# Kernel tuning notes

Hardware: AMD Instinct MI355X
Metric: run time of the kernel (lower is better)

## Reference

```python
import jax, jax.numpy as jnp
import numpy as np

B, N = 4, 1024
D_MODEL, N_HEADS, D_HEAD, D_COORD = 512, 8, 64, 2


def setup_inputs() -> dict:
    key = jax.random.key(0)
    ks = jax.random.split(key, 8)
    sd = 1.0 / np.sqrt(D_MODEL)
    return {
        "x": jax.random.normal(ks[0], (B, N, D_MODEL), dtype=jnp.float32),
        "positions": jax.random.uniform(ks[1], (N, D_COORD), dtype=jnp.float32) * 32.0,
        "W_Q": jax.random.normal(ks[2], (D_MODEL, N_HEADS * D_HEAD), dtype=jnp.float32) * sd,
        "W_K": jax.random.normal(ks[3], (D_MODEL, N_HEADS * D_HEAD), dtype=jnp.float32) * sd,
        "W_V": jax.random.normal(ks[4], (D_MODEL, N_HEADS * D_HEAD), dtype=jnp.float32) * sd,
        "W_O": jax.random.normal(ks[5], (N_HEADS * D_HEAD, D_MODEL), dtype=jnp.float32) * sd,
        "U": jax.random.normal(ks[6], (N_HEADS, D_HEAD, D_HEAD), dtype=jnp.float32),
        "freqs": jax.random.normal(ks[7], (N_HEADS, D_HEAD // 2, D_COORD), dtype=jnp.float32),
    }


def reference(x, positions, W_Q, W_K, W_V, W_O, U, freqs):
    # x: (B,N,d_model); positions: (N,d_coord); U: (H,dh,dh); freqs: (H,m,d_coord)
    Bn, Nn, _ = x.shape
    H, dh, _ = U.shape
    m = dh // 2
    scale = (dh // 2) ** -0.5

    Q = (x @ W_Q).reshape(Bn, Nn, H, dh)
    K = (x @ W_K).reshape(Bn, Nn, H, dh)
    V = (x @ W_V).reshape(Bn, Nn, H, dh)

    # Active-subspace projector: Pi = qr(U)[0] @ qr(U)[0].T per head
    Uq = jax.vmap(lambda u: jnp.linalg.qr(u)[0])(U)              # (H,dh,dh)
    P = jnp.einsum('hde,hfe->hdf', Uq, Uq)                       # U U^T
    Qp = jnp.einsum('bnhd,hdf->bhnf', Q, P)                      # (B,H,N,dh)
    Kp = jnp.einsum('bnhd,hdf->bhnf', K, P)

    # Relative rotation: R_rel(r_j - r_i) is block-diag 2x2 rotations with
    # angle theta_ijm = freqs_m . (r_j - r_i) = a_jm - a_im (separable), so
    # q^T R(r_j-r_i) k = (R(a_i)q)^T (R(a_j)k)  -- exact RoPE identity.
    ang = jnp.einsum('nc,hmc->hnm', positions, freqs)            # (H,N,m)
    c = jnp.cos(ang)[None]                                       # (1,H,N,m)
    s = jnp.sin(ang)[None]

    def rot(v):  # v: (B,H,N,dh) -> rotated (even, odd) halves (B,H,N,m)
        ve, vo = v[..., ::2], v[..., 1::2]
        return ve * c - vo * s, ve * s + vo * c

    qe, qo = rot(Qp)
    ke, ko = rot(Kp)
    scores = (jnp.einsum('bhim,bhjm->bhij', qe, ke)
              + jnp.einsum('bhim,bhjm->bhij', qo, ko)) * scale   # (B,H,N,N)
    w = jax.nn.softmax(scores, axis=-1)
    out = jnp.einsum('bhij,bjhd->bihd', w, V).reshape(Bn, Nn, H * dh)
    return out @ W_O
```

## Files before the change

### kernel.cpp

```cpp
#include <hip/hip_runtime.h>
#include <hip/hip_bf16.h>
#include <math.h>

#define NBATCH 4
#define NSEQ   1024
#define DMODEL 512
#define NH     8
#define DH     64
#define MROWS  (NBATCH*NSEQ)
#define MHALF  (DH/2)

typedef __attribute__((ext_vector_type(8))) short bf16x8;
typedef __attribute__((ext_vector_type(4))) float floatx4;

__device__ __forceinline__ uint f2bf2(float lo, float hi) {
    union { __hip_bfloat162 h; uint u; } v;
    v.h = __float22bfloat162_rn(make_float2(lo, hi));
    return v.u;
}

__global__ __launch_bounds__(256) void prep_kernel(
    const float* __restrict__ pos, const float* __restrict__ freqs,
    const float* __restrict__ x,
    const float* __restrict__ Wq, const float* __restrict__ Wk,
    const float* __restrict__ Wv, const float* __restrict__ Wo,
    float* __restrict__ cosT, float* __restrict__ sinT,
    ushort* __restrict__ xb, ushort* __restrict__ Wt)
{
    __shared__ float T[64][65];
    const int bid = blockIdx.x;
    const int tid = threadIdx.x;

    if (bid < 1024) {
        int idx = bid * 256 + tid;
        int m = idx & 31;
        int n = (idx >> 5) & 1023;
        int h = idx >> 15;
        float a = pos[n*2+0] * freqs[(h*MHALF+m)*2+0]
                + pos[n*2+1] * freqs[(h*MHALF+m)*2+1];
        cosT[idx] = cosf(a);
        sinT[idx] = sinf(a);
    } else if (bid < 2048) {
        int idx = ((bid - 1024) * 256 + tid) * 8;
        float4 a = *(const float4*)&x[idx];
        float4 b = *(const float4*)&x[idx+4];
        uint4 pk;
        pk.x = f2bf2(a.x, a.y);
        pk.y = f2bf2(a.z, a.w);
        pk.z = f2bf2(b.x, b.y);
        pk.w = f2bf2(b.z, b.w);
        *(uint4*)&xb[idx] = pk;
    } else {
        int b2 = bid - 2048;
        int n0g = (b2 & 31) * 64;
        int k0  = (b2 >> 5) * 64;
        int mat = n0g >> 9;
        const float* W = (mat == 0) ? Wq : ((mat == 1) ? Wk : ((mat == 2) ? Wv : Wo));
        int n0 = n0g & 511;
        int c = tid & 63, r = tid >> 6;
        #pragma unroll
        for (int i = 0; i < 16; i++)
            T[r + i*4][c] = W[(k0 + r + i*4) * DMODEL + n0 + c];
        __syncthreads();
        int nl = tid >> 2;
        int kg = tid & 3;
        #pragma unroll
        for (int g = 0; g < 4; g++) {
            int kl = kg * 16 + g * 4;
            uint2 pk;
            pk.x = f2bf2(T[kl+0][nl], T[kl+1][nl]);
            pk.y = f2bf2(T[kl+2][nl], T[kl+3][nl]);
            *(uint2*)&Wt[(size_t)(n0g + nl) * DMODEL + k0 + kl] = pk;
        }
    }
}

__global__ __launch_bounds__(256) void qkv_gemm(
    const ushort* __restrict__ xb, const ushort* __restrict__ Wt,
    const float* __restrict__ cosT, const float* __restrict__ sinT,
    ushort* __restrict__ Qb, ushort* __restrict__ Kb, ushort* __restrict__ Vt)
{
    __shared__ __align__(16) ushort AB[2 * 64 * 72];
    ushort* As = AB;
    ushort* Bs = AB + 64 * 72;
    float (*Cs)[65] = (float(*)[65])AB;

    const int cb = blockIdx.x;
    const int rb = blockIdx.y;
    const int mat = cb >> 3;
    const int c0 = (cb & 7) * 64;
    const int r0 = rb * 64;
    const int ng0 = mat * 512 + c0;

    const int tid = threadIdx.x;
    const int w = tid >> 6, l = tid & 63;
    const int lr = l & 15, lg = l >> 4;

    const int srow = tid >> 2;
    const int scol = (tid & 3) * 16;

    floatx4 acc[4];
    #pragma unroll
    for (int nt = 0; nt < 4; nt++) acc[nt] = (floatx4){0.f,0.f,0.f,0.f};

    const ushort* pa = &xb[(size_t)(r0 + srow) * DMODEL + scol];
    const ushort* pb = &Wt[(size_t)(ng0 + srow) * DMODEL + scol];
    uint4 ra0 = *(const uint4*)pa;
    uint4 ra1 = *(const uint4*)(pa + 8);
    uint4 rb0 = *(const uint4*)pb;
    uint4 rb1 = *(const uint4*)(pb + 8);

    for (int k0 = 0; k0 < DMODEL; k0 += 64) {
        __syncthreads();
        *(uint4*)&As[srow*72 + scol]     = ra0;
        *(uint4*)&As[srow*72 + scol + 8] = ra1;
        *(uint4*)&Bs[srow*72 + scol]     = rb0;
        *(uint4*)&Bs[srow*72 + scol + 8] = rb1;
        __syncthreads();

        if (k0 + 64 < DMODEL) {
            const ushort* na = &xb[(size_t)(r0 + srow) * DMODEL + k0 + 64 + scol];
            const ushort* nb = &Wt[(size_t)(ng0 + srow) * DMODEL + k0 + 64 + scol];
            ra0 = *(const uint4*)na;
            ra1 = *(const uint4*)(na + 8);
            rb0 = *(const uint4*)nb;
            rb1 = *(const uint4*)(nb + 8);
        }

        #pragma unroll
        for (int ks = 0; ks < 2; ks++) {
            bf16x8 af = *(const bf16x8*)&As[(16*w + lr)*72 + ks*32 + lg*8];
            #pragma unroll
            for (int nt = 0; nt < 4; nt++) {
                bf16x8 bf = *(const bf16x8*)&Bs[(nt*16 + lr)*72 + ks*32 + lg*8];
                acc[nt] = __builtin_amdgcn_mfma_f32_16x16x32_bf16(af, bf, acc[nt], 0, 0, 0);
            }
        }
    }

    __syncthreads();
    #pragma unroll
    for (int nt = 0; nt < 4; nt++)
        #pragma unroll
        for (int r = 0; r < 4; r++)
            Cs[16*w + lg*4 + r][nt*16 + lr] = acc[nt][r];
    __syncthreads();

    const int tx = tid & 15, ty = tid >> 4;
    const int dbase = tx * 4;
    const int head = c0 >> 6;

    if (mat == 2) {
        int rowbase = r0 + ty * 4;
        int b = rowbase >> 10, n0 = rowbase & 1023;
        size_t vbase = (size_t)(b * NH + head) * DH;
        #pragma unroll
        for (int j = 0; j < 4; j++) {
            uint2 pk;
            pk.x = f2bf2(Cs[ty*4 + 0][tx*4 + j], Cs[ty*4 + 1][tx*4 + j]);
            pk.y = f2bf2(Cs[ty*4 + 2][tx*4 + j], Cs[ty*4 + 3][tx*4 + j]);
            *(uint2*)&Vt[(vbase + dbase + j) * NSEQ + n0] = pk;
        }
    } else {
        ushort* dst = (mat == 0) ? Qb : Kb;
        const float qs = (mat == 0) ? 0.17677669529663687f : 1.0f;
        #pragma unroll
        for (int i = 0; i < 4; i++) {
            int row = r0 + ty * 4 + i;
            int b = row >> 10, n = row & 1023;
            float v[4];
            #pragma unroll
            for (int p = 0; p < 2; p++) {
                int de = dbase + 2 * p;
                int m = de >> 1;
                float c = cosT[(head * NSEQ + n) * MHALF + m] * qs;
                float s = sinT[(head * NSEQ + n) * MHALF + m] * qs;
                float ve = Cs[ty*4 + i][tx*4 + 2*p];
                float vo = Cs[ty*4 + i][tx*4 + 2*p + 1];
                v[2*p]     = ve * c - vo * s;
                v[2*p + 1] = ve * s + vo * c;
            }
            uint2 pk;
            pk.x = f2bf2(v[0], v[1]);
            pk.y = f2bf2(v[2], v[3]);
            *(uint2*)&dst[((size_t)(b * NH + head) * NSEQ + n) * DH + dbase] = pk;
        }
    }
}

__global__ __launch_bounds__(256, 4) void attn_kernel(
    const ushort* __restrict__ Qb, const ushort* __restrict__ Kb,
    const ushort* __restrict__ Vt, ushort* __restrict__ Obb)
{
    __shared__ ushort Ks[64 * 72];
    __shared__ ushort Vs[64 * 72];
    __shared__ ushort Ps[64 * 72];

    const int tid = threadIdx.x;
    const int w = tid >> 6, l = tid & 63;
    const int lr = l & 15, lg = l >> 4;
    const int bh = blockIdx.y, q0 = blockIdx.x * 64;

    const ushort* Qg = Qb + (size_t)bh * NSEQ * DH;
    const ushort* Kg = Kb + (size_t)bh * NSEQ * DH;
    const ushort* Vg = Vt + (size_t)bh * DH * NSEQ;

    bf16x8 qf[2];
    #pragma unroll
    for (int ks = 0; ks < 2; ks++)
        qf[ks] = *(const bf16x8*)(Qg + (size_t)(q0 + 16*w + lr) * DH + ks*32 + lg*8);

    floatx4 ot[4];
    #pragma unroll
    for (int i = 0; i < 4; i++) ot[i] = (floatx4){0.f, 0.f, 0.f, 0.f};
    float l_lane = 0.f;

    const int sr = tid >> 2;
    const int sc = (tid & 3) * 16;

    const ushort* kp = Kg + (size_t)sr * DH + sc;
    uint4 ka  = *(const uint4*)kp;
    uint4 kb2 = *(const uint4*)(kp + 8);
    const ushort* vp = Vg + (size_t)sr * NSEQ + sc;
    uint4 va  = *(const uint4*)vp;
    uint4 vb2 = *(const uint4*)(vp + 8);

    for (int jt = 0; jt < 16; jt++) {
        __syncthreads();
        *(uint4*)&Ks[sr*72 + sc]     = ka;
        *(uint4*)&Ks[sr*72 + sc + 8] = kb2;
        *(uint4*)&Vs[sr*72 + sc]     = va;
        *(uint4*)&Vs[sr*72 + sc + 8] = vb2;
        __syncthreads();

        if (jt < 15) {
            const ushort* kn = Kg + (size_t)((jt+1)*64 + sr) * DH + sc;
            ka  = *(const uint4*)kn;
            kb2 = *(const uint4*)(kn + 8);
            const ushort* vn = Vg + (size_t)sr * NSEQ + (jt+1)*64 + sc;
            va  = *(const uint4*)vn;
            vb2 = *(const uint4*)(vn + 8);
        }

        floatx4 st[4];
        #pragma unroll
        for (int jm = 0; jm < 4; jm++) {
            floatx4 acc = (floatx4){0.f, 0.f, 0.f, 0.f};
            #pragma unroll
            for (int ks = 0; ks < 2; ks++) {
                bf16x8 af = *(const bf16x8*)&Ks[(jm*16 + lr)*72 + ks*32 + lg*8];
                acc = __builtin_amdgcn_mfma_f32_16x16x32_bf16(af, qf[ks], acc, 0, 0, 0);
            }
            st[jm] = acc;
        }

        #pragma unroll
        for (int jm = 0; jm < 4; jm++) {
            float p0 = __expf(st[jm][0]);
            float p1 = __expf(st[jm][1]);
            float p2 = __expf(st[jm][2]);
            float p3 = __expf(st[jm][3]);
            l_lane += (p0 + p1) + (p2 + p3);
            uint2 pk;
            pk.x = f2bf2(p0, p1);
            pk.y = f2bf2(p2, p3);
            *(uint2*)&Ps[(16*w + lr)*72 + jm*16 + lg*4] = pk;
        }

        bf16x8 pf[2];
        #pragma unroll
        for (int ks = 0; ks < 2; ks++)
            pf[ks] = *(const bf16x8*)&Ps[(16*w + lr)*72 + ks*32 + lg*8];
        #pragma unroll
        for (int dt = 0; dt < 4; dt++)
            #pragma unroll
            for (int ks = 0; ks < 2; ks++) {
                bf16x8 af = *(const bf16x8*)&Vs[(dt*16 + lr)*72 + ks*32 + lg*8];
                ot[dt] = __builtin_amdgcn_mfma_f32_16x16x32_bf16(af, pf[ks], ot[dt], 0, 0, 0);
            }
    }

    l_lane += __shfl_xor(l_lane, 16, 64);
    l_lane += __shfl_xor(l_lane, 32, 64);
    float inv = 1.f / l_lane;

    int n = q0 + 16*w + lr;
    size_t obase = ((size_t)bh * NSEQ + n) * DH;
    #pragma unroll
    for (int dt = 0; dt < 4; dt++) {
        uint2 pk;
        pk.x = f2bf2(ot[dt][0] * inv, ot[dt][1] * inv);
        pk.y = f2bf2(ot[dt][2] * inv, ot[dt][3] * inv);
        *(uint2*)&Obb[obase + dt*16 + lg*4] = pk;
    }
}

__global__ __launch_bounds__(256) void out_gemm(
    const ushort* __restrict__ Obb, const ushort* __restrict__ Wt,
    float* __restrict__ out)
{
    __shared__ ushort As[64 * 40];
    __shared__ ushort Bs[64 * 40];
    __shared__ float  Cs[64][65];

    const int cb = blockIdx.x;
    const int rb = blockIdx.y;
    const int c0 = cb * 64, r0 = rb * 64;

    const int tid = threadIdx.x;
    const int w = tid >> 6, l = tid & 63;
    const int lr = l & 15, lg = l >> 4;
    const int srow = tid >> 2;
    const int sgrp = tid & 3;

    const int arow = r0 + srow;
    const int b = arow >> 10, n = arow & 1023;

    floatx4 acc[4];
    #pragma unroll
    for (int nt = 0; nt < 4; nt++) acc[nt] = (floatx4){0.f,0.f,0.f,0.f};

    #define A_ADDR(K0) (&Obb[((size_t)(b*NH + ((K0) >> 6)) * NSEQ + n) * DH + ((K0) & 63) + sgrp*8])

    uint4 rav = *(const uint4*)A_ADDR(0);
    uint4 rbv = *(const uint4*)&Wt[(size_t)(1536 + c0 + srow) * DMODEL + sgrp*8];

    for (int k0 = 0; k0 < DMODEL; k0 += 32) {
        __syncthreads();
        *(uint4*)&As[srow*40 + sgrp*8] = rav;
        *(uint4*)&Bs[srow*40 + sgrp*8] = rbv;
        __syncthreads();

        if (k0 + 32 < DMODEL) {
            rav = *(const uint4*)A_ADDR(k0 + 32);
            rbv = *(const uint4*)&Wt[(size_t)(1536 + c0 + srow) * DMODEL + (k0 + 32) + sgrp*8];
        }

        bf16x8 af = *(const bf16x8*)&As[(16*w + lr)*40 + lg*8];
        #pragma unroll
        for (int nt = 0; nt < 4; nt++) {
            bf16x8 bf = *(const bf16x8*)&Bs[(nt*16 + lr)*40 + lg*8];
            acc[nt] = __builtin_amdgcn_mfma_f32_16x16x32_bf16(af, bf, acc[nt], 0, 0, 0);
        }
    }
    #undef A_ADDR

    __syncthreads();
    #pragma unroll
    for (int nt = 0; nt < 4; nt++)
        #pragma unroll
        for (int r = 0; r < 4; r++)
            Cs[16*w + lg*4 + r][nt*16 + lr] = acc[nt][r];
    __syncthreads();

    const int tx = tid & 15, ty = tid >> 4;
    #pragma unroll
    for (int i = 0; i < 4; i++) {
        float4 o;
        o.x = Cs[ty*4 + i][tx*4 + 0];
        o.y = Cs[ty*4 + i][tx*4 + 1];
        o.z = Cs[ty*4 + i][tx*4 + 2];
        o.w = Cs[ty*4 + i][tx*4 + 3];
        *(float4*)&out[(size_t)(r0 + ty*4 + i) * DMODEL + c0 + tx*4] = o;
    }
}

extern "C" void kernel_launch(void* const* d_in, const int* in_sizes, int n_in,
                              void* d_out, int out_size, void* d_ws, size_t ws_size,
                              hipStream_t stream) {
    const float* x         = (const float*)d_in[0];
    const float* positions = (const float*)d_in[1];
    const float* Wq        = (const float*)d_in[2];
    const float* Wk        = (const float*)d_in[3];
    const float* Wv        = (const float*)d_in[4];
    const float* Wo        = (const float*)d_in[5];
    const float* freqs     = (const float*)d_in[7];
    float* out = (float*)d_out;

    float*  ws    = (float*)d_ws;
    float*  cosT  = ws;
    float*  sinT  = cosT + NH*NSEQ*MHALF;
    ushort* xb    = (ushort*)(sinT + NH*NSEQ*MHALF);
    ushort* Wt    = xb + (size_t)MROWS*DMODEL;
    ushort* Qb    = Wt + (size_t)2048*DMODEL;
    ushort* Kb    = Qb + (size_t)NBATCH*NH*NSEQ*DH;
    ushort* Vt    = Kb + (size_t)NBATCH*NH*NSEQ*DH;
    ushort* Obb   = Vt + (size_t)NBATCH*NH*NSEQ*DH;

    prep_kernel<<<dim3(2304), 256, 0, stream>>>(positions, freqs, x, Wq, Wk, Wv, Wo,
                                                cosT, sinT, xb, Wt);
    qkv_gemm<<<dim3(24, 64), 256, 0, stream>>>(xb, Wt, cosT, sinT, Qb, Kb, Vt);
    attn_kernel<<<dim3(16, 32), 256, 0, stream>>>(Qb, Kb, Vt, Obb);
    out_gemm<<<dim3(8, 64), 256, 0, stream>>>(Obb, Wt, out);
}
```

Before: 124.1 us.

## Split attention key dimension across warps with 32-query tiles and LDS reduction

The attention kernel now handles 32 queries per block instead of 64, and the four warps split into two query slices times two key halves. Each warp computes half of each key tile's scores and PV products, and the partial outputs and row sums are combined through shared memory at the end. This doubles the grid to 1024 blocks for better occupancy and CU coverage. The cost is that K/V tiles are loaded twice as often per query, plus an extra reduction and synchronisation.

```diff
diff --git a/kernel.cpp b/kernel.cpp
--- a/kernel.cpp
+++ b/kernel.cpp
@@ -163,7 +163,7 @@
         }
     } else {
         ushort* dst = (mat == 0) ? Qb : Kb;
-        const float qs = (mat == 0) ? 0.17677669529663687f : 1.0f;
+        const float qs2 = (mat == 0) ? 0.17677669529663687f : 1.0f;
         #pragma unroll
         for (int i = 0; i < 4; i++) {
             int row = r0 + ty * 4 + i;
@@ -173,8 +173,8 @@
             for (int p = 0; p < 2; p++) {
                 int de = dbase + 2 * p;
                 int m = de >> 1;
-                float c = cosT[(head * NSEQ + n) * MHALF + m] * qs;
-                float s = sinT[(head * NSEQ + n) * MHALF + m] * qs;
+                float c = cosT[(head * NSEQ + n) * MHALF + m] * qs2;
+                float s = sinT[(head * NSEQ + n) * MHALF + m] * qs2;
                 float ve = Cs[ty*4 + i][tx*4 + 2*p];
                 float vo = Cs[ty*4 + i][tx*4 + 2*p + 1];
                 v[2*p]     = ve * c - vo * s;
@@ -192,14 +192,17 @@
     const ushort* __restrict__ Qb, const ushort* __restrict__ Kb,
     const ushort* __restrict__ Vt, ushort* __restrict__ Obb)
 {
-    __shared__ ushort Ks[64 * 72];
-    __shared__ ushort Vs[64 * 72];
-    __shared__ ushort Ps[64 * 72];
+    __shared__ __align__(16) ushort S[2*64*72 + 32*72];
+    ushort* Ks = S;
+    ushort* Vs = S + 64*72;
+    ushort* Ps = S + 2*64*72;
 
     const int tid = threadIdx.x;
     const int w = tid >> 6, l = tid & 63;
     const int lr = l & 15, lg = l >> 4;
-    const int bh = blockIdx.y, q0 = blockIdx.x * 64;
+    const int qs = w & 1;
+    const int jh = w >> 1;
+    const int bh = blockIdx.y, q0 = blockIdx.x * 32;
 
     const ushort* Qg = Qb + (size_t)bh * NSEQ * DH;
     const ushort* Kg = Kb + (size_t)bh * NSEQ * DH;
@@ -208,7 +211,7 @@
     bf16x8 qf[2];
     #pragma unroll
     for (int ks = 0; ks < 2; ks++)
-        qf[ks] = *(const bf16x8*)(Qg + (size_t)(q0 + 16*w + lr) * DH + ks*32 + lg*8);
+        qf[ks] = *(const bf16x8*)(Qg + (size_t)(q0 + 16*qs + lr) * DH + ks*32 + lg*8);
 
     floatx4 ot[4];
     #pragma unroll
@@ -242,56 +245,62 @@
             vb2 = *(const uint4*)(vn + 8);
         }
 
-        floatx4 st[4];
-        #pragma unroll
-        for (int jm = 0; jm < 4; jm++) {
+        #pragma unroll
+        for (int jm2 = 0; jm2 < 2; jm2++) {
+            const int jm = jh*2 + jm2;
             floatx4 acc = (floatx4){0.f, 0.f, 0.f, 0.f};
             #pragma unroll
             for (int ks = 0; ks < 2; ks++) {
                 bf16x8 af = *(const bf16x8*)&Ks[(jm*16 + lr)*72 + ks*32 + lg*8];
                 acc = __builtin_amdgcn_mfma_f32_16x16x32_bf16(af, qf[ks], acc, 0, 0, 0);
             }
-            st[jm] = acc;
-        }
-
-        #pragma unroll
-        for (int jm = 0; jm < 4; jm++) {
-            float p0 = __expf(st[jm][0]);
-            float p1 = __expf(st[jm][1]);
-            float p2 = __expf(st[jm][2]);
-            float p3 = __expf(st[jm][3]);
+            float p0 = __expf(acc[0]);
+            float p1 = __expf(acc[1]);
+            float p2 = __expf(acc[2]);
+            float p3 = __expf(acc[3]);
             l_lane += (p0 + p1) + (p2 + p3);
             uint2 pk;
             pk.x = f2bf2(p0, p1);
             pk.y = f2bf2(p2, p3);
-            *(uint2*)&Ps[(16*w + lr)*72 + jm*16 + lg*4] = pk;
-        }
-
-        bf16x8 pf[2];
-        #pragma unroll
-        for (int ks = 0; ks < 2; ks++)
-            pf[ks] = *(const bf16x8*)&Ps[(16*w + lr)*72 + ks*32 + lg*8];
-        #pragma unroll
-        for (int dt = 0; dt < 4; dt++)
+            *(uint2*)&Ps[(16*qs + lr)*72 + jm*16 + lg*4] = pk;
+        }
+
+        {
+            bf16x8 pf = *(const bf16x8*)&Ps[(16*qs + lr)*72 + jh*32 + lg*8];
             #pragma unroll
-            for (int ks = 0; ks < 2; ks++) {
-                bf16x8 af = *(const bf16x8*)&Vs[(dt*16 + lr)*72 + ks*32 + lg*8];
-                ot[dt] = __builtin_amdgcn_mfma_f32_16x16x32_bf16(af, pf[ks], ot[dt], 0, 0, 0);
+            for (int dt = 0; dt < 4; dt++) {
+                bf16x8 af = *(const bf16x8*)&Vs[(dt*16 + lr)*72 + jh*32 + lg*8];
+                ot[dt] = __builtin_amdgcn_mfma_f32_16x16x32_bf16(af, pf, ot[dt], 0, 0, 0);
             }
+        }
     }
 
     l_lane += __shfl_xor(l_lane, 16, 64);
     l_lane += __shfl_xor(l_lane, 32, 64);
-    float inv = 1.f / l_lane;
-
-    int n = q0 + 16*w + lr;
-    size_t obase = ((size_t)bh * NSEQ + n) * DH;
-    #pragma unroll
-    for (int dt = 0; dt < 4; dt++) {
-        uint2 pk;
-        pk.x = f2bf2(ot[dt][0] * inv, ot[dt][1] * inv);
-        pk.y = f2bf2(ot[dt][2] * inv, ot[dt][3] * inv);
-        *(uint2*)&Obb[obase + dt*16 + lg*4] = pk;
+
+    __syncthreads();
+    float* Os = (float*)S;
+    float* Ls = (float*)(S + 5120);
+    if (w >= 2) {
+        #pragma unroll
+        for (int dt = 0; dt < 4; dt++)
+            *(float4*)&Os[(qs*64 + l)*20 + dt*4] = *(float4*)&ot[dt];
+        if (lg == 0) Ls[qs*16 + lr] = l_lane;
+    }
+    __syncthreads();
+    if (w < 2) {
+        float lsum = l_lane + Ls[qs*16 + lr];
+        float inv = 1.f / lsum;
+        int n = q0 + 16*qs + lr;
+        size_t obase = ((size_t)bh * NSEQ + n) * DH;
+        #pragma unroll
+        for (int dt = 0; dt < 4; dt++) {
+            float4 p = *(const float4*)&Os[(qs*64 + l)*20 + dt*4];
+            uint2 pk;
+            pk.x = f2bf2((ot[dt][0] + p.x) * inv, (ot[dt][1] + p.y) * inv);
+            pk.y = f2bf2((ot[dt][2] + p.z) * inv, (ot[dt][3] + p.w) * inv);
+            *(uint2*)&Obb[obase + dt*16 + lg*4] = pk;
+        }
     }
 }
 
@@ -390,6 +399,6 @@
     prep_kernel<<<dim3(2304), 256, 0, stream>>>(positions, freqs, x, Wq, Wk, Wv, Wo,
                                                 cosT, sinT, xb, Wt);
     qkv_gemm<<<dim3(24, 64), 256, 0, stream>>>(xb, Wt, cosT, sinT, Qb, Kb, Vt);
-    attn_kernel<<<dim3(16, 32), 256, 0, stream>>>(Qb, Kb, Vt, Obb);
+    attn_kernel<<<dim3(32, 32), 256, 0, stream>>>(Qb, Kb, Vt, Obb);
     out_gemm<<<dim3(8, 64), 256, 0, stream>>>(Obb, Wt, out);
 }
```

Result: no change. 123.0 us (-0.9%).
